# Kernel optimization log

Hardware: AMD Instinct MI355X
Metric: run time of the kernel (lower is better)

Reference implementation:

```python
import jax, jax.numpy as jnp
import numpy as np
from jax import lax

WIN = 7
K1, K2 = 0.01, 0.03
NP_ = WIN * WIN
COV_NORM = NP_ / (NP_ - 1)


def _box_filter(t, w):
    # t: [B, C, H, W] -> valid 7x7 box mean, [B, C, H-6, W-6]
    B, C, H, W = t.shape
    o = lax.conv_general_dilated(
        t.reshape(B * C, 1, H, W), w, window_strides=(1, 1), padding='VALID',
        dimension_numbers=('NCHW', 'OIHW', 'NCHW'))
    return o.reshape(B, C, H - WIN + 1, W - WIN + 1)


def setup_inputs() -> dict:
    key = jax.random.key(0)
    kx, ky = jax.random.split(key)
    X = jax.random.uniform(kx, (32, 3, 512, 512), dtype=jnp.float32)
    Y = jax.random.uniform(ky, (32, 3, 512, 512), dtype=jnp.float32)
    return {"X": X, "Y": Y}


def reference(X, Y):
    data_range = 1.0
    C1 = (K1 * data_range) ** 2
    C2 = (K2 * data_range) ** 2
    w = jnp.full((1, 1, WIN, WIN), 1.0 / NP_, dtype=X.dtype)

    ux = _box_filter(X, w)
    uy = _box_filter(Y, w)
    uxx = _box_filter(X * X, w)
    uyy = _box_filter(Y * Y, w)
    uxy = _box_filter(X * Y, w)

    vx = COV_NORM * (uxx - ux * ux)
    vy = COV_NORM * (uyy - uy * uy)
    vxy = COV_NORM * (uxy - ux * uy)

    A1 = 2 * ux * uy + C1
    A2 = 2 * vxy + C2
    B1 = ux * ux + uy * uy + C1
    B2 = vx + vy + C2
    S = (A1 * A2) / (B1 * B2)
    # reduced=True: per-channel means then mean over channels == global mean
    # (all channels have identical spatial size)
    return 1.0 - jnp.mean(S)
```

## Files before the change

kernel.cpp:

```cpp
#include <hip/hip_runtime.h>


#define IW    512
#define OUTW  506
#define BAND  22
#define NBANDS 23
#define NIMG  96
#define NPART (NBANDS * NIMG)
#define C1N2  0.2401f
#define C2N2  2.1609f
#define KA    (49.0f/24.0f)
#define KB    (49.0f/48.0f)
#define TOTAL_OUT 24579456.0f

__device__ __forceinline__ float ssim_raw(float Sx, float Sy, float Sxx,
                                          float Syy, float Sxy) {
    float sxsy = Sx * Sy;
    float p    = fmaf(Sx, Sx, Sy * Sy);
    float a1   = fmaf(2.0f, sxsy, C1N2);
    float b1   = p + C1N2;
    float a2   = fmaf(KA, fmaf(49.0f, Sxy, -sxsy), C2N2);
    float b2   = fmaf(KB, fmaf(49.0f, Sxx + Syy, -p), C2N2);
    return (a1 * a2) * __builtin_amdgcn_rcpf(b1 * b2);
}

__global__ __launch_bounds__(256, 5) void ssim_main(const float* __restrict__ X,
                                                    const float* __restrict__ Y,
                                                    float* __restrict__ partials) {
    __shared__ float plane[2][5][65 * 12];
    __shared__ float wsum[4];

    const int t    = threadIdx.x;
    const int band = blockIdx.x;
    const int img  = blockIdx.y;
    const int r0   = band * BAND;
    const float2* X2 = (const float2*)(X + (size_t)img * IW * IW);
    const float2* Y2 = (const float2*)(Y + (size_t)img * IW * IW);

    float sxa=0,sxb=0, sya=0,syb=0, sxxa=0,sxxb=0, syya=0,syyb=0, sxya=0,sxyb=0;

#pragma unroll
    for (int i = 0; i < 6; ++i) {
        float2 x = X2[(r0 + i) * 256 + t];
        float2 y = Y2[(r0 + i) * 256 + t];
        sxa += x.x;  sxb += x.y;  sya += y.x;  syb += y.y;
        sxxa = fmaf(x.x,x.x,sxxa); sxxb = fmaf(x.y,x.y,sxxb);
        syya = fmaf(y.x,y.x,syya); syyb = fmaf(y.y,y.y,syyb);
        sxya = fmaf(x.x,y.x,sxya); sxyb = fmaf(x.y,y.y,sxyb);
    }

    const int woff = 12 * (t >> 2) + 2 * (t & 3);

    const int hw  = t >> 7;
    const int ht  = t & 127;
    const int p0  = 4 * ht;
    const int u   = ht >> 1;
    const int off = (ht & 1) * 4;
    const int aA = 12 * u + off;
    const int aB = 12 * u + (off ? 12 : 4);
    const int aC = 12 * u + 12 + off;

    float2 nx[2], ny[2], rx[2], ry[2];
#pragma unroll
    for (int k = 0; k < 2; ++k) {
        nx[k] = X2[(r0 + 6 + k) * 256 + t];
        ny[k] = Y2[(r0 + 6 + k) * 256 + t];
        rx[k] = X2[(r0 + k) * 256 + t];
        ry[k] = Y2[(r0 + k) * 256 + t];
    }

    float accS = 0.0f;

    for (int j = 0; j < BAND; j += 2) {
#pragma unroll
        for (int k = 0; k < 2; ++k) {
            float2 x = nx[k], y = ny[k];
            sxa += x.x;  sxb += x.y;  sya += y.x;  syb += y.y;
            sxxa = fmaf(x.x,x.x,sxxa); sxxb = fmaf(x.y,x.y,sxxb);
            syya = fmaf(y.x,y.x,syya); syyb = fmaf(y.y,y.y,syyb);
            sxya = fmaf(x.x,y.x,sxya); sxyb = fmaf(x.y,y.y,sxyb);
            *(float2*)&plane[k][0][woff] = make_float2(sxa,  sxb);
            *(float2*)&plane[k][1][woff] = make_float2(sya,  syb);
            *(float2*)&plane[k][2][woff] = make_float2(sxxa, sxxb);
            *(float2*)&plane[k][3][woff] = make_float2(syya, syyb);
            *(float2*)&plane[k][4][woff] = make_float2(sxya, sxyb);
            float2 ox = rx[k], oy = ry[k];
            sxa -= ox.x;  sxb -= ox.y;  sya -= oy.x;  syb -= oy.y;
            sxxa = fmaf(-ox.x,ox.x,sxxa); sxxb = fmaf(-ox.y,ox.y,sxxb);
            syya = fmaf(-oy.x,oy.x,syya); syyb = fmaf(-oy.y,oy.y,syyb);
            sxya = fmaf(-ox.x,oy.x,sxya); sxyb = fmaf(-ox.y,oy.y,sxyb);
        }
        __syncthreads();

        if (j + 2 < BAND) {
#pragma unroll
            for (int k = 0; k < 2; ++k) {
                nx[k] = X2[(r0 + j + 8 + k) * 256 + t];
                ny[k] = Y2[(r0 + j + 8 + k) * 256 + t];
                rx[k] = X2[(r0 + j + 2 + k) * 256 + t];
                ry[k] = Y2[(r0 + j + 2 + k) * 256 + t];
            }
        }

        {
            float c[5][10];
#pragma unroll
            for (int q = 0; q < 5; ++q) {
                const float* pl = plane[hw][q];
                float4 A = *(const float4*)(pl + aA);
                float4 B = *(const float4*)(pl + aB);
                float2 C = *(const float2*)(pl + aC);
                c[q][0]=A.x; c[q][1]=A.y; c[q][2]=A.z; c[q][3]=A.w;
                c[q][4]=B.x; c[q][5]=B.y; c[q][6]=B.z; c[q][7]=B.w;
                c[q][8]=C.x; c[q][9]=C.y;
            }
            float W[5];
#pragma unroll
            for (int q = 0; q < 5; ++q)
                W[q] = ((c[q][0] + c[q][1]) + (c[q][2] + c[q][3])) +
                       ((c[q][4] + c[q][5]) + c[q][6]);
            accS += (p0 < OUTW) ? ssim_raw(W[0],W[1],W[2],W[3],W[4]) : 0.0f;
#pragma unroll
            for (int m = 1; m < 4; ++m) {
#pragma unroll
                for (int q = 0; q < 5; ++q)
                    W[q] += c[q][m + 6] - c[q][m - 1];
                float Sv = ssim_raw(W[0],W[1],W[2],W[3],W[4]);
                accS += (p0 + m < OUTW) ? Sv : 0.0f;
            }
        }
        __syncthreads();
    }

#pragma unroll
    for (int o = 32; o > 0; o >>= 1)
        accS += __shfl_down(accS, o, 64);
    if ((t & 63) == 0) wsum[t >> 6] = accS;
    __syncthreads();
    if (t == 0)
        partials[blockIdx.y * NBANDS + blockIdx.x] =
            (wsum[0] + wsum[1]) + (wsum[2] + wsum[3]);
}

__global__ __launch_bounds__(256) void ssim_finalize(const float* __restrict__ partials,
                                                     float* __restrict__ out) {
    __shared__ float wsum[4];
    const int t = threadIdx.x;
    float v = 0.0f;
    for (int i = t; i < NPART; i += 256) v += partials[i];
#pragma unroll
    for (int o = 32; o > 0; o >>= 1)
        v += __shfl_down(v, o, 64);
    if ((t & 63) == 0) wsum[t >> 6] = v;
    __syncthreads();
    if (t == 0)
        out[0] = 1.0f - ((wsum[0] + wsum[1]) + (wsum[2] + wsum[3])) / TOTAL_OUT;
}

extern "C" void kernel_launch(void* const* d_in, const int* in_sizes, int n_in,
                              void* d_out, int out_size, void* d_ws, size_t ws_size,
                              hipStream_t stream) {
    const float* X = (const float*)d_in[0];
    const float* Y = (const float*)d_in[1];
    float* partials = (float*)d_ws;
    float* out = (float*)d_out;

    hipLaunchKernelGGL(ssim_main, dim3(NBANDS, NIMG), dim3(256), 0, stream,
                       X, Y, partials);
    hipLaunchKernelGGL(ssim_finalize, dim3(1), dim3(256), 0, stream,
                       partials, out);
}
```

Measured before the change: 228.4 us.

## Replace LDS horizontal window with per-wave register sums and lane shuffles

```diff
diff --git a/kernel.cpp b/kernel.cpp
--- a/kernel.cpp
+++ b/kernel.cpp
@@ -3,143 +3,144 @@
 
 #define IW    512
 #define OUTW  506
-#define BAND  22
-#define NBANDS 23
+#define BAND  11
+#define NBANDS 46
 #define NIMG  96
-#define NPART (NBANDS * NIMG)
+#define WPB   4
+#define NBLK  (NBANDS * NIMG / WPB)
+#define NPART NBLK
 #define C1N2  0.2401f
 #define C2N2  2.1609f
 #define KA    (49.0f/24.0f)
 #define KB    (49.0f/48.0f)
 #define TOTAL_OUT 24579456.0f
 
-__device__ __forceinline__ float ssim_raw(float Sx, float Sy, float Sxx,
-                                          float Syy, float Sxy) {
+__device__ __forceinline__ float ssim_raw(float Sx, float Sy, float S2, float Sxy) {
     float sxsy = Sx * Sy;
     float p    = fmaf(Sx, Sx, Sy * Sy);
     float a1   = fmaf(2.0f, sxsy, C1N2);
     float b1   = p + C1N2;
     float a2   = fmaf(KA, fmaf(49.0f, Sxy, -sxsy), C2N2);
-    float b2   = fmaf(KB, fmaf(49.0f, Sxx + Syy, -p), C2N2);
+    float b2   = fmaf(KB, fmaf(49.0f, S2, -p), C2N2);
     return (a1 * a2) * __builtin_amdgcn_rcpf(b1 * b2);
 }
 
-__global__ __launch_bounds__(256, 5) void ssim_main(const float* __restrict__ X,
+__device__ __forceinline__ void unpack8(float4 a, float4 b, float* d) {
+    d[0]=a.x; d[1]=a.y; d[2]=a.z; d[3]=a.w;
+    d[4]=b.x; d[5]=b.y; d[6]=b.z; d[7]=b.w;
+}
+
+__global__ __launch_bounds__(256, 4) void ssim_main(const float* __restrict__ X,
                                                     const float* __restrict__ Y,
                                                     float* __restrict__ partials) {
-    __shared__ float plane[2][5][65 * 12];
-    __shared__ float wsum[4];
+    __shared__ float wsum[WPB];
+    const int t    = threadIdx.x;
+    const int wv   = t >> 6;
+    const int lane = t & 63;
+    const int gw   = blockIdx.x * WPB + wv;
+    const int img  = gw / NBANDS;
+    const int band = gw - img * NBANDS;
+    const int r0   = band * BAND;
+    const float4* X4 = (const float4*)X + (size_t)img * (IW * IW / 4);
+    const float4* Y4 = (const float4*)Y + (size_t)img * (IW * IW / 4);
+    const int c0 = 2 * lane;
 
-    const int t    = threadIdx.x;
-    const int band = blockIdx.x;
-    const int img  = blockIdx.y;
-    const int r0   = band * BAND;
-    const float2* X2 = (const float2*)(X + (size_t)img * IW * IW);
-    const float2* Y2 = (const float2*)(Y + (size_t)img * IW * IW);
-
-    float sxa=0,sxb=0, sya=0,syb=0, sxxa=0,sxxb=0, syya=0,syyb=0, sxya=0,sxyb=0;
+    float sx[8], sy[8], s2[8], sxy[8];
+#pragma unroll
+    for (int q = 0; q < 8; ++q) { sx[q]=0.f; sy[q]=0.f; s2[q]=0.f; sxy[q]=0.f; }
 
 #pragma unroll
     for (int i = 0; i < 6; ++i) {
-        float2 x = X2[(r0 + i) * 256 + t];
-        float2 y = Y2[(r0 + i) * 256 + t];
-        sxa += x.x;  sxb += x.y;  sya += y.x;  syb += y.y;
-        sxxa = fmaf(x.x,x.x,sxxa); sxxb = fmaf(x.y,x.y,sxxb);
-        syya = fmaf(y.x,y.x,syya); syyb = fmaf(y.y,y.y,syyb);
-        sxya = fmaf(x.x,y.x,sxya); sxyb = fmaf(x.y,y.y,sxyb);
+        const int ro = (r0 + i) * (IW / 4);
+        float4 xa = X4[ro + c0], xb = X4[ro + c0 + 1];
+        float4 ya = Y4[ro + c0], yb = Y4[ro + c0 + 1];
+        float x[8], y[8];
+        unpack8(xa, xb, x); unpack8(ya, yb, y);
+#pragma unroll
+        for (int q = 0; q < 8; ++q) {
+            sx[q] += x[q]; sy[q] += y[q];
+            s2[q]  = fmaf(x[q], x[q], s2[q]);
+            s2[q]  = fmaf(y[q], y[q], s2[q]);
+            sxy[q] = fmaf(x[q], y[q], sxy[q]);
+        }
     }
 
-    const int woff = 12 * (t >> 2) + 2 * (t & 3);
-
-    const int hw  = t >> 7;
-    const int ht  = t & 127;
-    const int p0  = 4 * ht;
-    const int u   = ht >> 1;
-    const int off = (ht & 1) * 4;
-    const int aA = 12 * u + off;
-    const int aB = 12 * u + (off ? 12 : 4);
-    const int aC = 12 * u + 12 + off;
-
-    float2 nx[2], ny[2], rx[2], ry[2];
-#pragma unroll
-    for (int k = 0; k < 2; ++k) {
-        nx[k] = X2[(r0 + 6 + k) * 256 + t];
-        ny[k] = Y2[(r0 + 6 + k) * 256 + t];
-        rx[k] = X2[(r0 + k) * 256 + t];
-        ry[k] = Y2[(r0 + k) * 256 + t];
-    }
+    int rn = (r0 + 6) * (IW / 4);
+    float4 nxa = X4[rn + c0], nxb = X4[rn + c0 + 1];
+    float4 nya = Y4[rn + c0], nyb = Y4[rn + c0 + 1];
 
     float accS = 0.0f;
 
-    for (int j = 0; j < BAND; j += 2) {
+#pragma unroll 1
+    for (int r = 0; r < BAND; ++r) {
+        {
+            float x[8], y[8];
+            unpack8(nxa, nxb, x); unpack8(nya, nyb, y);
 #pragma unroll
-        for (int k = 0; k < 2; ++k) {
-            float2 x = nx[k], y = ny[k];
-            sxa += x.x;  sxb += x.y;  sya += y.x;  syb += y.y;
-            sxxa = fmaf(x.x,x.x,sxxa); sxxb = fmaf(x.y,x.y,sxxb);
-            syya = fmaf(y.x,y.x,syya); syyb = fmaf(y.y,y.y,syyb);
-            sxya = fmaf(x.x,y.x,sxya); sxyb = fmaf(x.y,y.y,sxyb);
-            *(float2*)&plane[k][0][woff] = make_float2(sxa,  sxb);
-            *(float2*)&plane[k][1][woff] = make_float2(sya,  syb);
-            *(float2*)&plane[k][2][woff] = make_float2(sxxa, sxxb);
-            *(float2*)&plane[k][3][woff] = make_float2(syya, syyb);
-            *(float2*)&plane[k][4][woff] = make_float2(sxya, sxyb);
-            float2 ox = rx[k], oy = ry[k];
-            sxa -= ox.x;  sxb -= ox.y;  sya -= oy.x;  syb -= oy.y;
-            sxxa = fmaf(-ox.x,ox.x,sxxa); sxxb = fmaf(-ox.y,ox.y,sxxb);
-            syya = fmaf(-oy.x,oy.x,syya); syyb = fmaf(-oy.y,oy.y,syyb);
-            sxya = fmaf(-ox.x,oy.x,sxya); sxyb = fmaf(-ox.y,oy.y,sxyb);
+            for (int q = 0; q < 8; ++q) {
+                sx[q] += x[q]; sy[q] += y[q];
+                s2[q]  = fmaf(x[q], x[q], s2[q]);
+                s2[q]  = fmaf(y[q], y[q], s2[q]);
+                sxy[q] = fmaf(x[q], y[q], sxy[q]);
+            }
         }
-        __syncthreads();
+        const int rr = (r0 + r) * (IW / 4);
+        float4 rxa = X4[rr + c0], rxb = X4[rr + c0 + 1];
+        float4 rya = Y4[rr + c0], ryb = Y4[rr + c0 + 1];
+        rn = ((r < BAND - 1) ? (r0 + 7 + r) : (r0 + 6)) * (IW / 4);
+        nxa = X4[rn + c0]; nxb = X4[rn + c0 + 1];
+        nya = Y4[rn + c0]; nyb = Y4[rn + c0 + 1];
 
-        if (j + 2 < BAND) {
+        float Wx[8], Wy[8], W2[8], Wxy[8];
+#define HWIN(S, W)                                                         \
+        {                                                                  \
+            float h0 = __shfl_down(S[0], 1, 64);                           \
+            float h1 = __shfl_down(S[1], 1, 64);                           \
+            float h2 = __shfl_down(S[2], 1, 64);                           \
+            float h3 = __shfl_down(S[3], 1, 64);                           \
+            float h4 = __shfl_down(S[4], 1, 64);                           \
+            float h5 = __shfl_down(S[5], 1, 64);                           \
+            W[0] = ((S[0]+S[1]) + (S[2]+S[3])) + ((S[4]+S[5]) + S[6]);     \
+            W[1] = W[0] + (S[7] - S[0]);                                   \
+            W[2] = W[1] + (h0   - S[1]);                                   \
+            W[3] = W[2] + (h1   - S[2]);                                   \
+            W[4] = W[3] + (h2   - S[3]);                                   \
+            W[5] = W[4] + (h3   - S[4]);                                   \
+            W[6] = W[5] + (h4   - S[5]);                                   \
+            W[7] = W[6] + (h5   - S[6]);                                   \
+        }
+        HWIN(sx,  Wx)
+        HWIN(sy,  Wy)
+        HWIN(s2,  W2)
+        HWIN(sxy, Wxy)
+#undef HWIN
+
 #pragma unroll
-            for (int k = 0; k < 2; ++k) {
-                nx[k] = X2[(r0 + j + 8 + k) * 256 + t];
-                ny[k] = Y2[(r0 + j + 8 + k) * 256 + t];
-                rx[k] = X2[(r0 + j + 2 + k) * 256 + t];
-                ry[k] = Y2[(r0 + j + 2 + k) * 256 + t];
-            }
+        for (int m = 0; m < 8; ++m) {
+            float Sv = ssim_raw(Wx[m], Wy[m], W2[m], Wxy[m]);
+            accS += (8 * lane + m < OUTW) ? Sv : 0.0f;
         }
 
         {
-            float c[5][10];
+            float x[8], y[8];
+            unpack8(rxa, rxb, x); unpack8(rya, ryb, y);
 #pragma unroll
-            for (int q = 0; q < 5; ++q) {
-                const float* pl = plane[hw][q];
-                float4 A = *(const float4*)(pl + aA);
-                float4 B = *(const float4*)(pl + aB);
-                float2 C = *(const float2*)(pl + aC);
-                c[q][0]=A.x; c[q][1]=A.y; c[q][2]=A.z; c[q][3]=A.w;
-                c[q][4]=B.x; c[q][5]=B.y; c[q][6]=B.z; c[q][7]=B.w;
-                c[q][8]=C.x; c[q][9]=C.y;
-            }
-            float W[5];
-#pragma unroll
-            for (int q = 0; q < 5; ++q)
-                W[q] = ((c[q][0] + c[q][1]) + (c[q][2] + c[q][3])) +
-                       ((c[q][4] + c[q][5]) + c[q][6]);
-            accS += (p0 < OUTW) ? ssim_raw(W[0],W[1],W[2],W[3],W[4]) : 0.0f;
-#pragma unroll
-            for (int m = 1; m < 4; ++m) {
-#pragma unroll
-                for (int q = 0; q < 5; ++q)
-                    W[q] += c[q][m + 6] - c[q][m - 1];
-                float Sv = ssim_raw(W[0],W[1],W[2],W[3],W[4]);
-                accS += (p0 + m < OUTW) ? Sv : 0.0f;
+            for (int q = 0; q < 8; ++q) {
+                sx[q] -= x[q]; sy[q] -= y[q];
+                s2[q]  = fmaf(-x[q], x[q], s2[q]);
+                s2[q]  = fmaf(-y[q], y[q], s2[q]);
+                sxy[q] = fmaf(-x[q], y[q], sxy[q]);
             }
         }
-        __syncthreads();
     }
 
 #pragma unroll
     for (int o = 32; o > 0; o >>= 1)
         accS += __shfl_down(accS, o, 64);
-    if ((t & 63) == 0) wsum[t >> 6] = accS;
+    if (lane == 0) wsum[wv] = accS;
     __syncthreads();
     if (t == 0)
-        partials[blockIdx.y * NBANDS + blockIdx.x] =
-            (wsum[0] + wsum[1]) + (wsum[2] + wsum[3]);
+        partials[blockIdx.x] = (wsum[0] + wsum[1]) + (wsum[2] + wsum[3]);
 }
 
 __global__ __launch_bounds__(256) void ssim_finalize(const float* __restrict__ partials,
@@ -165,7 +166,7 @@
     float* partials = (float*)d_ws;
     float* out = (float*)d_out;
 
-    hipLaunchKernelGGL(ssim_main, dim3(NBANDS, NIMG), dim3(256), 0, stream,
+    hipLaunchKernelGGL(ssim_main, dim3(NBLK), dim3(256), 0, stream,
                        X, Y, partials);
     hipLaunchKernelGGL(ssim_finalize, dim3(1), dim3(256), 0, stream,
                        partials, out);
```

Result: slower. 246.5 us (+7.9%).
